# Optimization experiments

Hardware: AMD Instinct MI355X
Metric: run time of the kernel (lower is better)

Reference implementation:

```python
import jax, jax.numpy as jnp
import numpy as np

N, IN_DIM, OUT_DIM = 8192, 512, 256
ALPHA = 0.2  # LeakyReLU negative slope
MASK_VAL = -9e15


def setup_inputs() -> dict:
    key = jax.random.key(0)
    k1, k2, k3, k4 = jax.random.split(key, 4)
    inp = jax.random.normal(k1, (N, IN_DIM), dtype=jnp.float32)
    adj = jax.random.randint(k2, (N, N), 0, 2, dtype=jnp.int32)
    # xavier-ish scaled params
    weight = jax.random.normal(k3, (IN_DIM, OUT_DIM), dtype=jnp.float32) * (2.0 / (IN_DIM + OUT_DIM)) ** 0.5
    a = jax.random.normal(k4, (2 * OUT_DIM, 1), dtype=jnp.float32) * (2.0 / (2 * OUT_DIM + 1)) ** 0.5
    return {"input": inp, "adj": adj, "weight": weight, "a": a}


def reference(input, adj, weight, a):
    Wh = input @ weight                        # [N, D_out]
    Wh1 = Wh @ a[:OUT_DIM, :]                  # [N, 1]
    Wh2 = Wh @ a[OUT_DIM:, :]                  # [N, 1]
    e = Wh1 + Wh2.T                            # [N, N] broadcast additive score
    e = jnp.where(e > 0, e, ALPHA * e)         # LeakyReLU
    e = jnp.where(adj > 0, e, MASK_VAL)        # adjacency mask
    attention = jax.nn.softmax(e, axis=-1)     # [N, N]
    # dropout p=0.0 -> identity
    out = attention @ Wh                       # [N, D_out]
    return jax.nn.elu(out)
```

## Files before the change

kernel.cpp:

```cpp
#include <hip/hip_runtime.h>
#include <hip/hip_bf16.h>
#include <stdint.h>

#define NN 8192
#define DIN 512
#define DOUT 256
#define NSPLIT 4
#define STRIP (NN / NSPLIT)

typedef short short8 __attribute__((ext_vector_type(8)));
typedef float floatx4 __attribute__((ext_vector_type(4)));

__device__ __forceinline__ unsigned short f2bf_rne(float x) {
  unsigned u = __float_as_uint(x);
  u += 0x7fffu + ((u >> 16) & 1u);
  return (unsigned short)(u >> 16);
}
__device__ __forceinline__ float bf2f(unsigned short h) {
  return __uint_as_float(((unsigned)h) << 16);
}

__global__ __launch_bounds__(256) void kt_transpose(const float* __restrict__ Wg,
                                                    unsigned short* __restrict__ WT) {
  __shared__ unsigned short sm[32][33];
  int tid = threadIdx.x;
  int bk = blockIdx.x >> 3;
  int bn = blockIdx.x & 7;
  int k0 = bk * 32, n0 = bn * 32;
  int r = tid >> 3, c4 = (tid & 7) * 4;
  const float* src = Wg + (size_t)(k0 + r) * DOUT + n0 + c4;
#pragma unroll
  for (int x = 0; x < 4; ++x) sm[r][c4 + x] = f2bf_rne(src[x]);
  __syncthreads();
  unsigned short* dst = WT + (size_t)(n0 + r) * DIN + k0 + c4;
#pragma unroll
  for (int x = 0; x < 4; ++x) dst[x] = sm[c4 + x][r];
}

__global__ __launch_bounds__(256) void kt_gemm1(const float* __restrict__ X,
                                                const unsigned short* __restrict__ WT,
                                                const float* __restrict__ Ab,
                                                unsigned short* __restrict__ WhT,
                                                float* __restrict__ Wh1,
                                                float* __restrict__ Wh2) {
  int tid = threadIdx.x;
  int w = tid >> 6, lane = tid & 63;
  int col = lane & 15, q = lane >> 4;
  int db = blockIdx.x & 3;
  int ib = blockIdx.x >> 2;
  int i0 = ib * 128;
  int drow = db * 64 + w * 16 + col;
  const unsigned short* abase = WT + (size_t)drow * DIN + q * 8;
  const float* xbase = X + (size_t)(i0 + col) * DIN + q * 8;
  floatx4 acc[8];
#pragma unroll
  for (int t = 0; t < 8; ++t) acc[t] = (floatx4)(0.0f);
  for (int k0 = 0; k0 < DIN; k0 += 32) {
    short8 af = *(const short8*)(abase + k0);
#pragma unroll
    for (int t = 0; t < 8; ++t) {
      const float* xp = xbase + (size_t)t * 16 * DIN + k0;
      float4 xa = *(const float4*)xp;
      float4 xb = *(const float4*)(xp + 4);
      short8 bf;
      bf[0] = (short)f2bf_rne(xa.x); bf[1] = (short)f2bf_rne(xa.y);
      bf[2] = (short)f2bf_rne(xa.z); bf[3] = (short)f2bf_rne(xa.w);
      bf[4] = (short)f2bf_rne(xb.x); bf[5] = (short)f2bf_rne(xb.y);
      bf[6] = (short)f2bf_rne(xb.z); bf[7] = (short)f2bf_rne(xb.w);
      acc[t] = __builtin_amdgcn_mfma_f32_16x16x32_bf16(af, bf, acc[t], 0, 0, 0);
    }
  }
  int dq = db * 64 + w * 16 + q * 4;
  float a1v[4], a2v[4];
#pragma unroll
  for (int r = 0; r < 4; ++r) { a1v[r] = Ab[dq + r]; a2v[r] = Ab[DOUT + dq + r]; }
#pragma unroll
  for (int t = 0; t < 8; ++t) {
    floatx4 v = acc[t];
    int icol = i0 + t * 16 + col;
#pragma unroll
    for (int r = 0; r < 4; ++r) WhT[(size_t)(dq + r) * NN + icol] = f2bf_rne(v[r]);
    float p1 = v[0] * a1v[0] + v[1] * a1v[1] + v[2] * a1v[2] + v[3] * a1v[3];
    float p2 = v[0] * a2v[0] + v[1] * a2v[1] + v[2] * a2v[2] + v[3] * a2v[3];
    p1 += __shfl_xor(p1, 16);
    p1 += __shfl_xor(p1, 32);
    p2 += __shfl_xor(p2, 16);
    p2 += __shfl_xor(p2, 32);
    if (q == 0) {
      atomicAdd(&Wh1[icol], p1);
      atomicAdd(&Wh2[icol], p2);
    }
  }
}

__device__ __forceinline__ short8 build_a(int4 pa, int4 pb, float wh1, const float* w2,
                                          float& lsum) {
  int av[8] = {pa.x, pa.y, pa.z, pa.w, pb.x, pb.y, pb.z, pb.w};
  short8 af;
#pragma unroll
  for (int e = 0; e < 8; ++e) {
    float sc = wh1 + w2[e];
    sc = fmaxf(sc, 0.2f * sc);
    float ex = __expf(sc);
    float wv = (av[e] != 0) ? ex : 0.0f;
    unsigned short hb = f2bf_rne(wv);
    af[e] = (short)hb;
    lsum += bf2f(hb);
  }
  return af;
}

__global__ __launch_bounds__(256, 2) void kt_attn(const int* __restrict__ adj,
                                                  const unsigned short* __restrict__ WhT,
                                                  const float* __restrict__ Wh1,
                                                  const float* __restrict__ Wh2,
                                                  float* __restrict__ accg,
                                                  float* __restrict__ lg) {
  __shared__ __align__(16) unsigned short tileB[32 * DOUT];
  __shared__ __align__(16) float wh2s[STRIP];
  int tid = threadIdx.x;
  int w = tid >> 6, lane = tid & 63;
  int col = lane & 15, q = lane >> 4;
  int s = blockIdx.x & (NSPLIT - 1);
  int ib = blockIdx.x / NSPLIT;
  int i0 = ib * 64;
  int jb = s * STRIP;
  int wr = (w >> 1) * 32;
  int dh = (w & 1) * 128;

  for (int t = tid; t < STRIP / 4; t += 256)
    ((floatx4*)wh2s)[t] = ((const floatx4*)(Wh2 + jb))[t];

  float wh1r0 = Wh1[i0 + wr + col];
  float wh1r1 = Wh1[i0 + wr + 16 + col];

  int drow = tid;
  int fsw = (drow >> 1) & 3;
  const unsigned short* gsrc = WhT + (size_t)drow * NN + jb;
  unsigned short* lrow = &tileB[drow * 32];

  int fc = (col >> 1) & 3;
  const unsigned short* bbase = &tileB[(dh + col) * 32 + ((q ^ fc) * 8)];

  const int* aptr0 = adj + ((size_t)(i0 + wr + col) << 13) + jb + q * 8;
  const int* aptr1 = adj + ((size_t)(i0 + wr + 16 + col) << 13) + jb + q * 8;

  floatx4 acc[2][8];
#pragma unroll
  for (int g = 0; g < 2; ++g)
#pragma unroll
    for (int t = 0; t < 8; ++t) acc[g][t] = (floatx4)(0.0f);
  float lp0 = 0.f, lp1 = 0.f;

  short8 st[4];
#pragma unroll
  for (int m = 0; m < 4; ++m) st[m] = *(const short8*)(gsrc + m * 8);
  int4 ad0a = *(const int4*)aptr0;
  int4 ad0b = *(const int4*)(aptr0 + 4);
  int4 ad1a = *(const int4*)aptr1;
  int4 ad1b = *(const int4*)(aptr1 + 4);

  const int NSTEP = STRIP / 32;
#pragma unroll 1
  for (int k = 0; k < NSTEP; ++k) {
    int jl = k * 32;
    __syncthreads();
#pragma unroll
    for (int m = 0; m < 4; ++m) *(short8*)(lrow + ((m ^ fsw) * 8)) = st[m];
    __syncthreads();
    if (k + 1 < NSTEP) {
#pragma unroll
      for (int m = 0; m < 4; ++m) st[m] = *(const short8*)(gsrc + (jl + 32) + m * 8);
    }
    short8 bf[8];
#pragma unroll
    for (int t = 0; t < 8; ++t) bf[t] = *(const short8*)(bbase + t * 512);
    floatx4 w2a = *(const floatx4*)&wh2s[jl + q * 8];
    floatx4 w2b = *(const floatx4*)&wh2s[jl + q * 8 + 4];
    float w2[8] = {w2a[0], w2a[1], w2a[2], w2a[3], w2b[0], w2b[1], w2b[2], w2b[3]};
    short8 af0 = build_a(ad0a, ad0b, wh1r0, w2, lp0);
    short8 af1 = build_a(ad1a, ad1b, wh1r1, w2, lp1);
    if (k + 1 < NSTEP) {
      ad0a = *(const int4*)(aptr0 + jl + 32);
      ad0b = *(const int4*)(aptr0 + jl + 36);
      ad1a = *(const int4*)(aptr1 + jl + 32);
      ad1b = *(const int4*)(aptr1 + jl + 36);
    }
#pragma unroll
    for (int t = 0; t < 8; ++t)
      acc[0][t] = __builtin_amdgcn_mfma_f32_16x16x32_bf16(af0, bf[t], acc[0][t], 0, 0, 0);
#pragma unroll
    for (int t = 0; t < 8; ++t)
      acc[1][t] = __builtin_amdgcn_mfma_f32_16x16x32_bf16(af1, bf[t], acc[1][t], 0, 0, 0);
  }

  lp0 += __shfl_xor(lp0, 16);
  lp0 += __shfl_xor(lp0, 32);
  lp1 += __shfl_xor(lp1, 16);
  lp1 += __shfl_xor(lp1, 32);
  if (((w & 1) == 0) && lane < 16) {
    atomicAdd(&lg[i0 + wr + lane], lp0);
    atomicAdd(&lg[i0 + wr + 16 + lane], lp1);
  }
#pragma unroll
  for (int g = 0; g < 2; ++g) {
#pragma unroll
    for (int t = 0; t < 8; ++t) {
      floatx4 v = acc[g][t];
      int dcol = dh + t * 16 + col;
      int irow = i0 + wr + g * 16 + q * 4;
#pragma unroll
      for (int r = 0; r < 4; ++r) atomicAdd(&accg[(size_t)(irow + r) * DOUT + dcol], v[r]);
    }
  }
}

__global__ __launch_bounds__(256) void kt_merge(const float* __restrict__ accg,
                                               const float* __restrict__ lg,
                                               float* __restrict__ out) {
  int i = blockIdx.x;
  int d = threadIdx.x;
  size_t idx = (size_t)i * DOUT + d;
  float x = accg[idx] / lg[i];
  x = x > 0.f ? x : (__expf(x) - 1.f);
  out[idx] = x;
}

extern "C" void kernel_launch(void* const* d_in, const int* in_sizes, int n_in,
                              void* d_out, int out_size, void* d_ws, size_t ws_size,
                              hipStream_t stream) {
  const float* X = (const float*)d_in[0];
  const int* adj = (const int*)d_in[1];
  const float* Wg = (const float*)d_in[2];
  const float* Ab = (const float*)d_in[3];
  float* out = (float*)d_out;

  char* ws = (char*)d_ws;
  float* accg = (float*)ws;
  size_t off = (size_t)NN * DOUT * 4;
  float* lg = (float*)(ws + off);  off += (size_t)NN * 4;
  float* Wh1 = (float*)(ws + off); off += (size_t)NN * 4;
  float* Wh2 = (float*)(ws + off); off += (size_t)NN * 4;
  size_t zero_bytes = off;
  unsigned short* WT = (unsigned short*)(ws + off);
  off += (size_t)DOUT * DIN * 2;
  unsigned short* WhT = (unsigned short*)(ws + off);
  off += (size_t)DOUT * NN * 2;

  hipMemsetAsync(accg, 0, zero_bytes, stream);
  kt_transpose<<<128, 256, 0, stream>>>(Wg, WT);
  kt_gemm1<<<256, 256, 0, stream>>>(X, WT, Ab, WhT, Wh1, Wh2);
  kt_attn<<<(NN / 64) * NSPLIT, 256, 0, stream>>>(adj, WhT, Wh1, Wh2, accg, lg);
  kt_merge<<<NN, 256, 0, stream>>>(accg, lg, out);
}
```

Before: 534.0 us.

## Retile attention kernel with double-buffered LDS, prepack X to bf16, exp2 scores

The attention kernel now gives each block 128 rows across the full 256-wide output, with 32 rows per wave. It splits the columns into 8 strips, double-buffers the WhT tile in LDS so one barrier per step is removed, and reads Wh2 straight from global memory. Exp is replaced by exp2 with log2e folded into the attention vector, and bf16 packing uses v_cvt_pk_bf16. X is converted to bf16 in a separate kernel before GEMM1, and GEMM1 is retiled to 64 rows per block. The merge kernel is vectorised. The tradeoffs are more accumulator registers per wave, an extra pass over X, and more atomic traffic from the extra column splits.

```diff
diff --git a/kernel.cpp b/kernel.cpp
--- a/kernel.cpp
+++ b/kernel.cpp
@@ -5,8 +5,10 @@
 #define NN 8192
 #define DIN 512
 #define DOUT 256
-#define NSPLIT 4
+#define NSPLIT 8
 #define STRIP (NN / NSPLIT)
+#define NSTEP (STRIP / 32)
+#define LOG2E 1.4426950408889634f
 
 typedef short short8 __attribute__((ext_vector_type(8)));
 typedef float floatx4 __attribute__((ext_vector_type(4)));
@@ -16,8 +18,11 @@
   u += 0x7fffu + ((u >> 16) & 1u);
   return (unsigned short)(u >> 16);
 }
-__device__ __forceinline__ float bf2f(unsigned short h) {
-  return __uint_as_float(((unsigned)h) << 16);
+
+__device__ __forceinline__ unsigned cvt_pk_bf16(float lo, float hi) {
+  unsigned r;
+  asm("v_cvt_pk_bf16_f32 %0, %1, %2" : "=v"(r) : "v"(lo), "v"(hi));
+  return r;
 }
 
 __global__ __launch_bounds__(256) void kt_transpose(const float* __restrict__ Wg,
@@ -37,7 +42,20 @@
   for (int x = 0; x < 4; ++x) dst[x] = sm[c4 + x][r];
 }
 
-__global__ __launch_bounds__(256) void kt_gemm1(const float* __restrict__ X,
+__global__ __launch_bounds__(256) void kt_cvtx(const float* __restrict__ X,
+                                               unsigned short* __restrict__ Xb) {
+  int g = blockIdx.x * 256 + threadIdx.x;
+  const float4* p = (const float4*)(X + (size_t)g * 8);
+  float4 a = p[0], b = p[1];
+  union { unsigned u[4]; short8 s8; } r;
+  r.u[0] = cvt_pk_bf16(a.x, a.y);
+  r.u[1] = cvt_pk_bf16(a.z, a.w);
+  r.u[2] = cvt_pk_bf16(b.x, b.y);
+  r.u[3] = cvt_pk_bf16(b.z, b.w);
+  *(short8*)(Xb + (size_t)g * 8) = r.s8;
+}
+
+__global__ __launch_bounds__(256) void kt_gemm1(const unsigned short* __restrict__ Xb,
                                                 const unsigned short* __restrict__ WT,
                                                 const float* __restrict__ Ab,
                                                 unsigned short* __restrict__ WhT,
@@ -46,36 +64,32 @@
   int tid = threadIdx.x;
   int w = tid >> 6, lane = tid & 63;
   int col = lane & 15, q = lane >> 4;
-  int db = blockIdx.x & 3;
-  int ib = blockIdx.x >> 2;
-  int i0 = ib * 128;
+  int ib = blockIdx.x & 127;
+  int db = blockIdx.x >> 7;
+  int i0 = ib * 64;
   int drow = db * 64 + w * 16 + col;
   const unsigned short* abase = WT + (size_t)drow * DIN + q * 8;
-  const float* xbase = X + (size_t)(i0 + col) * DIN + q * 8;
-  floatx4 acc[8];
-#pragma unroll
-  for (int t = 0; t < 8; ++t) acc[t] = (floatx4)(0.0f);
+  const unsigned short* xbase = Xb + (size_t)(i0 + col) * DIN + q * 8;
+  floatx4 acc[4];
+#pragma unroll
+  for (int t = 0; t < 4; ++t) acc[t] = (floatx4)(0.0f);
   for (int k0 = 0; k0 < DIN; k0 += 32) {
     short8 af = *(const short8*)(abase + k0);
 #pragma unroll
-    for (int t = 0; t < 8; ++t) {
-      const float* xp = xbase + (size_t)t * 16 * DIN + k0;
-      float4 xa = *(const float4*)xp;
-      float4 xb = *(const float4*)(xp + 4);
-      short8 bf;
-      bf[0] = (short)f2bf_rne(xa.x); bf[1] = (short)f2bf_rne(xa.y);
-      bf[2] = (short)f2bf_rne(xa.z); bf[3] = (short)f2bf_rne(xa.w);
-      bf[4] = (short)f2bf_rne(xb.x); bf[5] = (short)f2bf_rne(xb.y);
-      bf[6] = (short)f2bf_rne(xb.z); bf[7] = (short)f2bf_rne(xb.w);
+    for (int t = 0; t < 4; ++t) {
+      short8 bf = *(const short8*)(xbase + (size_t)t * 16 * DIN + k0);
       acc[t] = __builtin_amdgcn_mfma_f32_16x16x32_bf16(af, bf, acc[t], 0, 0, 0);
     }
   }
   int dq = db * 64 + w * 16 + q * 4;
   float a1v[4], a2v[4];
 #pragma unroll
-  for (int r = 0; r < 4; ++r) { a1v[r] = Ab[dq + r]; a2v[r] = Ab[DOUT + dq + r]; }
-#pragma unroll
-  for (int t = 0; t < 8; ++t) {
+  for (int r = 0; r < 4; ++r) {
+    a1v[r] = Ab[dq + r] * LOG2E;
+    a2v[r] = Ab[DOUT + dq + r] * LOG2E;
+  }
+#pragma unroll
+  for (int t = 0; t < 4; ++t) {
     floatx4 v = acc[t];
     int icol = i0 + t * 16 + col;
 #pragma unroll
@@ -93,21 +107,26 @@
   }
 }
 
-__device__ __forceinline__ short8 build_a(int4 pa, int4 pb, float wh1, const float* w2,
-                                          float& lsum) {
+__device__ __forceinline__ short8 build_a(int4 pa, int4 pb, float wh1, floatx4 w2a,
+                                          floatx4 w2b, float& lsum) {
   int av[8] = {pa.x, pa.y, pa.z, pa.w, pb.x, pb.y, pb.z, pb.w};
-  short8 af;
+  float w2[8] = {w2a[0], w2a[1], w2a[2], w2a[3], w2b[0], w2b[1], w2b[2], w2b[3]};
+  float wv[8];
 #pragma unroll
   for (int e = 0; e < 8; ++e) {
     float sc = wh1 + w2[e];
     sc = fmaxf(sc, 0.2f * sc);
-    float ex = __expf(sc);
-    float wv = (av[e] != 0) ? ex : 0.0f;
-    unsigned short hb = f2bf_rne(wv);
-    af[e] = (short)hb;
-    lsum += bf2f(hb);
-  }
-  return af;
+    float ex = __builtin_amdgcn_exp2f(sc);
+    wv[e] = (av[e] != 0) ? ex : 0.0f;
+  }
+  union { unsigned u[4]; short8 s8; } r;
+#pragma unroll
+  for (int p = 0; p < 4; ++p) {
+    unsigned pk = cvt_pk_bf16(wv[2 * p], wv[2 * p + 1]);
+    r.u[p] = pk;
+    lsum += __uint_as_float(pk << 16) + __uint_as_float(pk & 0xffff0000u);
+  }
+  return r.s8;
 }
 
 __global__ __launch_bounds__(256, 2) void kt_attn(const int* __restrict__ adj,
@@ -116,114 +135,120 @@
                                                   const float* __restrict__ Wh2,
                                                   float* __restrict__ accg,
                                                   float* __restrict__ lg) {
-  __shared__ __align__(16) unsigned short tileB[32 * DOUT];
-  __shared__ __align__(16) float wh2s[STRIP];
+  __shared__ __align__(16) unsigned short tileB[2][DOUT * 32];
   int tid = threadIdx.x;
   int w = tid >> 6, lane = tid & 63;
   int col = lane & 15, q = lane >> 4;
   int s = blockIdx.x & (NSPLIT - 1);
-  int ib = blockIdx.x / NSPLIT;
-  int i0 = ib * 64;
+  int ib = blockIdx.x >> 3;
+  int i0 = ib * 128;
   int jb = s * STRIP;
-  int wr = (w >> 1) * 32;
-  int dh = (w & 1) * 128;
-
-  for (int t = tid; t < STRIP / 4; t += 256)
-    ((floatx4*)wh2s)[t] = ((const floatx4*)(Wh2 + jb))[t];
-
-  float wh1r0 = Wh1[i0 + wr + col];
-  float wh1r1 = Wh1[i0 + wr + 16 + col];
-
-  int drow = tid;
-  int fsw = (drow >> 1) & 3;
-  const unsigned short* gsrc = WhT + (size_t)drow * NN + jb;
-  unsigned short* lrow = &tileB[drow * 32];
+
+  int r0 = i0 + w * 32 + col;
+  float wh1r0 = Wh1[r0];
+  float wh1r1 = Wh1[r0 + 16];
+
+  int fsw = (tid >> 1) & 3;
+  const unsigned short* gsrc = WhT + (size_t)tid * NN + jb;
+  unsigned short* lrow0 = &tileB[0][tid * 32];
 
   int fc = (col >> 1) & 3;
-  const unsigned short* bbase = &tileB[(dh + col) * 32 + ((q ^ fc) * 8)];
-
-  const int* aptr0 = adj + ((size_t)(i0 + wr + col) << 13) + jb + q * 8;
-  const int* aptr1 = adj + ((size_t)(i0 + wr + 16 + col) << 13) + jb + q * 8;
-
-  floatx4 acc[2][8];
-#pragma unroll
-  for (int g = 0; g < 2; ++g)
-#pragma unroll
-    for (int t = 0; t < 8; ++t) acc[g][t] = (floatx4)(0.0f);
+  const unsigned short* bb0 = &tileB[0][col * 32 + ((q ^ fc) * 8)];
+
+  const int* aptr0 = adj + ((size_t)r0 << 13) + jb + q * 8;
+  const int* aptr1 = adj + ((size_t)(r0 + 16) << 13) + jb + q * 8;
+  const float* wp = Wh2 + jb + q * 8;
+
+  floatx4 acc0[16], acc1[16];
+#pragma unroll
+  for (int t = 0; t < 16; ++t) {
+    acc0[t] = (floatx4)(0.0f);
+    acc1[t] = (floatx4)(0.0f);
+  }
   float lp0 = 0.f, lp1 = 0.f;
 
   short8 st[4];
 #pragma unroll
   for (int m = 0; m < 4; ++m) st[m] = *(const short8*)(gsrc + m * 8);
-  int4 ad0a = *(const int4*)aptr0;
-  int4 ad0b = *(const int4*)(aptr0 + 4);
-  int4 ad1a = *(const int4*)aptr1;
-  int4 ad1b = *(const int4*)(aptr1 + 4);
-
-  const int NSTEP = STRIP / 32;
+  int4 a0a = *(const int4*)aptr0;
+  int4 a0b = *(const int4*)(aptr0 + 4);
+  int4 a1a = *(const int4*)aptr1;
+  int4 a1b = *(const int4*)(aptr1 + 4);
+  floatx4 w2a = *(const floatx4*)wp;
+  floatx4 w2b = *(const floatx4*)(wp + 4);
+
 #pragma unroll 1
   for (int k = 0; k < NSTEP; ++k) {
-    int jl = k * 32;
-    __syncthreads();
-#pragma unroll
-    for (int m = 0; m < 4; ++m) *(short8*)(lrow + ((m ^ fsw) * 8)) = st[m];
+    int bsel = (k & 1) * (DOUT * 32);
+    unsigned short* lw = lrow0 + bsel;
+#pragma unroll
+    for (int m = 0; m < 4; ++m) *(short8*)(lw + ((m ^ fsw) * 8)) = st[m];
     __syncthreads();
     if (k + 1 < NSTEP) {
-#pragma unroll
-      for (int m = 0; m < 4; ++m) st[m] = *(const short8*)(gsrc + (jl + 32) + m * 8);
-    }
-    short8 bf[8];
-#pragma unroll
-    for (int t = 0; t < 8; ++t) bf[t] = *(const short8*)(bbase + t * 512);
-    floatx4 w2a = *(const floatx4*)&wh2s[jl + q * 8];
-    floatx4 w2b = *(const floatx4*)&wh2s[jl + q * 8 + 4];
-    float w2[8] = {w2a[0], w2a[1], w2a[2], w2a[3], w2b[0], w2b[1], w2b[2], w2b[3]};
-    short8 af0 = build_a(ad0a, ad0b, wh1r0, w2, lp0);
-    short8 af1 = build_a(ad1a, ad1b, wh1r1, w2, lp1);
+      const unsigned short* gs = gsrc + (size_t)(k + 1) * 32;
+#pragma unroll
+      for (int m = 0; m < 4; ++m) st[m] = *(const short8*)(gs + m * 8);
+    }
+    short8 af0 = build_a(a0a, a0b, wh1r0, w2a, w2b, lp0);
+    short8 af1 = build_a(a1a, a1b, wh1r1, w2a, w2b, lp1);
     if (k + 1 < NSTEP) {
-      ad0a = *(const int4*)(aptr0 + jl + 32);
-      ad0b = *(const int4*)(aptr0 + jl + 36);
-      ad1a = *(const int4*)(aptr1 + jl + 32);
-      ad1b = *(const int4*)(aptr1 + jl + 36);
-    }
-#pragma unroll
-    for (int t = 0; t < 8; ++t)
-      acc[0][t] = __builtin_amdgcn_mfma_f32_16x16x32_bf16(af0, bf[t], acc[0][t], 0, 0, 0);
-#pragma unroll
-    for (int t = 0; t < 8; ++t)
-      acc[1][t] = __builtin_amdgcn_mfma_f32_16x16x32_bf16(af1, bf[t], acc[1][t], 0, 0, 0);
+      int jn = (k + 1) * 32;
+      a0a = *(const int4*)(aptr0 + jn);
+      a0b = *(const int4*)(aptr0 + jn + 4);
+      a1a = *(const int4*)(aptr1 + jn);
+      a1b = *(const int4*)(aptr1 + jn + 4);
+      w2a = *(const floatx4*)(wp + jn);
+      w2b = *(const floatx4*)(wp + jn + 4);
+    }
+    const unsigned short* br = bb0 + bsel;
+#pragma unroll
+    for (int h = 0; h < 4; ++h) {
+      short8 bf[4];
+#pragma unroll
+      for (int t = 0; t < 4; ++t) bf[t] = *(const short8*)(br + (h * 4 + t) * 512);
+#pragma unroll
+      for (int t = 0; t < 4; ++t) {
+        acc0[h * 4 + t] =
+            __builtin_amdgcn_mfma_f32_16x16x32_bf16(af0, bf[t], acc0[h * 4 + t], 0, 0, 0);
+        acc1[h * 4 + t] =
+            __builtin_amdgcn_mfma_f32_16x16x32_bf16(af1, bf[t], acc1[h * 4 + t], 0, 0, 0);
+      }
+    }
   }
 
   lp0 += __shfl_xor(lp0, 16);
   lp0 += __shfl_xor(lp0, 32);
   lp1 += __shfl_xor(lp1, 16);
   lp1 += __shfl_xor(lp1, 32);
-  if (((w & 1) == 0) && lane < 16) {
-    atomicAdd(&lg[i0 + wr + lane], lp0);
-    atomicAdd(&lg[i0 + wr + 16 + lane], lp1);
-  }
-#pragma unroll
-  for (int g = 0; g < 2; ++g) {
-#pragma unroll
-    for (int t = 0; t < 8; ++t) {
-      floatx4 v = acc[g][t];
-      int dcol = dh + t * 16 + col;
-      int irow = i0 + wr + g * 16 + q * 4;
-#pragma unroll
-      for (int r = 0; r < 4; ++r) atomicAdd(&accg[(size_t)(irow + r) * DOUT + dcol], v[r]);
-    }
+  if (lane < 16) {
+    atomicAdd(&lg[i0 + w * 32 + lane], lp0);
+    atomicAdd(&lg[i0 + w * 32 + 16 + lane], lp1);
+  }
+#pragma unroll
+  for (int T = 0; T < 16; ++T) {
+    floatx4 v0 = acc0[T];
+    floatx4 v1 = acc1[T];
+    int dcol = T * 16 + col;
+    int irow0 = i0 + w * 32 + q * 4;
+#pragma unroll
+    for (int r = 0; r < 4; ++r) atomicAdd(&accg[(size_t)(irow0 + r) * DOUT + dcol], v0[r]);
+#pragma unroll
+    for (int r = 0; r < 4; ++r)
+      atomicAdd(&accg[(size_t)(irow0 + 16 + r) * DOUT + dcol], v1[r]);
   }
 }
 
 __global__ __launch_bounds__(256) void kt_merge(const float* __restrict__ accg,
-                                               const float* __restrict__ lg,
-                                               float* __restrict__ out) {
-  int i = blockIdx.x;
-  int d = threadIdx.x;
-  size_t idx = (size_t)i * DOUT + d;
-  float x = accg[idx] / lg[i];
-  x = x > 0.f ? x : (__expf(x) - 1.f);
-  out[idx] = x;
+                                                const float* __restrict__ lg,
+                                                float* __restrict__ out) {
+  int g = blockIdx.x * 256 + threadIdx.x;
+  int i = g >> 6;
+  float inv = 1.0f / lg[i];
+  float4 v = *(const float4*)(accg + (size_t)g * 4);
+  float o[4] = {v.x * inv, v.y * inv, v.z * inv, v.w * inv};
+#pragma unroll
+  for (int r = 0; r < 4; ++r) o[r] = o[r] > 0.f ? o[r] : (__expf(o[r]) - 1.f);
+  *(float4*)(out + (size_t)g * 4) = make_float4(o[0], o[1], o[2], o[3]);
 }
 
 extern "C" void kernel_launch(void* const* d_in, const int* in_sizes, int n_in,
@@ -237,19 +262,24 @@
 
   char* ws = (char*)d_ws;
   float* accg = (float*)ws;
+  unsigned short* Xb = (unsigned short*)ws;
   size_t off = (size_t)NN * DOUT * 4;
-  float* lg = (float*)(ws + off);  off += (size_t)NN * 4;
-  float* Wh1 = (float*)(ws + off); off += (size_t)NN * 4;
-  float* Wh2 = (float*)(ws + off); off += (size_t)NN * 4;
-  size_t zero_bytes = off;
+  float* lg = (float*)(ws + off);
+  off += (size_t)NN * 4;
+  float* Wh1 = (float*)(ws + off);
+  off += (size_t)NN * 4;
+  float* Wh2 = (float*)(ws + off);
+  off += (size_t)NN * 4;
   unsigned short* WT = (unsigned short*)(ws + off);
   off += (size_t)DOUT * DIN * 2;
   unsigned short* WhT = (unsigned short*)(ws + off);
   off += (size_t)DOUT * NN * 2;
 
-  hipMemsetAsync(accg, 0, zero_bytes, stream);
+  hipMemsetAsync(Wh1, 0, (size_t)NN * 8, stream);
+  kt_cvtx<<<2048, 256, 0, stream>>>(X, Xb);
   kt_transpose<<<128, 256, 0, stream>>>(Wg, WT);
-  kt_gemm1<<<256, 256, 0, stream>>>(X, WT, Ab, WhT, Wh1, Wh2);
-  kt_attn<<<(NN / 64) * NSPLIT, 256, 0, stream>>>(adj, WhT, Wh1, Wh2, accg, lg);
-  kt_merge<<<NN, 256, 0, stream>>>(accg, lg, out);
-}
+  kt_gemm1<<<512, 256, 0, stream>>>(Xb, WT, Ab, WhT, Wh1, Wh2);
+  hipMemsetAsync(ws, 0, (size_t)NN * DOUT * 4 + (size_t)NN * 4, stream);
+  kt_attn<<<(NN / 128) * NSPLIT, 256, 0, stream>>>(adj, WhT, Wh1, Wh2, accg, lg);
+  kt_merge<<<2048, 256, 0, stream>>>(accg, lg, out);
+}
```

Result: faster. 471.0 us (-11.8%).
